# Kernel tuning notes

Hardware: AMD Instinct MI355X
Metric: run time of the kernel (lower is better)

## Reference

```python
import jax, jax.numpy as jnp
import numpy as np

B, S, D = 4, 2048, 1024

def setup_inputs() -> dict:
    key = jax.random.key(0)
    k1, k2, k3, k4 = jax.random.split(key, 4)
    scale = 1.0 / np.sqrt(D)  # roughly glorot-like magnitude for weights
    return {
        "inputs": jax.random.normal(k1, (B, S, D), dtype=jnp.float32),
        "W_query": jax.random.normal(k2, (D, D), dtype=jnp.float32) * scale,
        "W_key": jax.random.normal(k3, (D, D), dtype=jnp.float32) * scale,
        "W_value": jax.random.normal(k4, (D, D), dtype=jnp.float32) * scale,
    }

def reference(inputs, W_query, W_key, W_value):
    # QKV projections: [B,S,D] @ [D,D]
    q = jnp.einsum('bsd,de->bse', inputs, W_query)
    k = jnp.einsum('bsd,de->bse', inputs, W_key)
    v = jnp.einsum('bsd,de->bse', inputs, W_value)
    # Unscaled attention scores [B,S,S] (source applies no 1/sqrt(d))
    score = jnp.einsum('bqd,bkd->bqk', q, k)
    weights = jax.nn.softmax(score, axis=-1)
    context = jnp.einsum('bqk,bkd->bqd', weights, v)
    return context
```

## Files before the change

### kernel.cpp

```cpp
#include <hip/hip_runtime.h>
#include <math.h>


typedef __bf16 bf16;
typedef _Float16 f16;
typedef __bf16 bf16x8 __attribute__((ext_vector_type(8)));
typedef __bf16 bf16x4 __attribute__((ext_vector_type(4)));
typedef _Float16 f16x4 __attribute__((ext_vector_type(4)));
typedef _Float16 f16x8 __attribute__((ext_vector_type(8)));
typedef float  f32x4  __attribute__((ext_vector_type(4)));

template<typename E> struct vec8_of;
template<> struct vec8_of<bf16> { using type = bf16x8; };
template<> struct vec8_of<f16>  { using type = f16x8; };

__device__ inline f32x4 mfma16(bf16x8 a, bf16x8 b, f32x4 c) {
    return __builtin_amdgcn_mfma_f32_16x16x32_bf16(a, b, c, 0, 0, 0);
}
__device__ inline f32x4 mfma16(f16x8 a, f16x8 b, f32x4 c) {
    return __builtin_amdgcn_mfma_f32_16x16x32_f16(a, b, c, 0, 0, 0);
}

#define AS1 __attribute__((address_space(1)))
#define AS3 __attribute__((address_space(3)))

template<typename E>
__device__ inline void async_load16(const E* g, void* l) {
    __builtin_amdgcn_global_load_lds((const AS1 unsigned int*)g,
                                     (AS3 unsigned int*)l, 16, 0, 0);
}

template<typename E, bool SPLIT, int OUT_MODE, int BK>
__global__ __launch_bounds__(256) void gemm_bt(
    const E* __restrict__ Ahi, const E* __restrict__ Alo,
    const E* __restrict__ Bhi, const E* __restrict__ Blo,
    float* __restrict__ Cf, f16* __restrict__ Ch,
    bf16* __restrict__ Cbh, bf16* __restrict__ Cbl,
    int K, int lda, int ldb, int ldc,
    long long sA, long long sB, long long sC)
{
    using vec8 = typename vec8_of<E>::type;
    constexpr int NBUF = SPLIT ? 4 : 2;
    constexpr int TILE_BYTES = 128 * BK * (int)sizeof(E);
    constexpr int CPW = (TILE_BYTES / 1024) / 4;
    constexpr int SPR = (BK * (int)sizeof(E)) / 16;
    constexpr int SWZ = (SPR == 8) ? 7 : 0;
    constexpr int SMB = (OUT_MODE == 2) ? (128 * 130 * 2 > NBUF * TILE_BYTES
                                           ? 128 * 130 * 2 : NBUF * TILE_BYTES)
                                        : NBUF * TILE_BYTES;

    __shared__ __align__(16) char smraw[SMB];
    auto tr = (f16(*)[130])smraw;

    Ahi += (long long)blockIdx.z * sA;
    Bhi += (long long)blockIdx.z * sB;
    if (SPLIT) { Alo += (long long)blockIdx.z * sA; Blo += (long long)blockIdx.z * sB; }

    const int tid  = threadIdx.x;
    const int lane = tid & 63;
    const int wave = tid >> 6;
    const int quad = lane >> 4;
    const int l16  = lane & 15;
    const int wm   = (wave >> 1) * 64;
    const int wn   = (wave & 1) * 64;

    const long long rowA0 = (long long)blockIdx.y * 128;
    const long long colB0 = (long long)blockIdx.x * 128;

    int ofs[CPW], rr[CPW], cc8[CPW];
#pragma unroll
    for (int u = 0; u < CPW; u++) {
        ofs[u] = (wave * CPW + u) * 1024 + lane * 16;
        const int s = ofs[u] >> 4;
        rr[u]  = s / SPR;
        cc8[u] = (s & (SPR - 1)) ^ (rr[u] & SWZ);
    }

    f32x4 acc[4][4];
#pragma unroll
    for (int i = 0; i < 4; i++)
#pragma unroll
        for (int j = 0; j < 4; j++) acc[i][j] = (f32x4){0.f, 0.f, 0.f, 0.f};

    for (int k0 = 0; k0 < K; k0 += BK) {
#pragma unroll
        for (int u = 0; u < CPW; u++) {
            async_load16(Ahi + (rowA0 + rr[u]) * lda + k0 + cc8[u] * 8, smraw + 0 * TILE_BYTES + ofs[u]);
            async_load16(Bhi + (colB0 + rr[u]) * ldb + k0 + cc8[u] * 8, smraw + 1 * TILE_BYTES + ofs[u]);
            if (SPLIT) {
                async_load16(Alo + (rowA0 + rr[u]) * lda + k0 + cc8[u] * 8, smraw + 2 * TILE_BYTES + ofs[u]);
                async_load16(Blo + (colB0 + rr[u]) * ldb + k0 + cc8[u] * 8, smraw + 3 * TILE_BYTES + ofs[u]);
            }
        }
        __syncthreads();

#pragma unroll
        for (int kh = 0; kh < BK / 32; kh++) {
            const int kc8 = kh * 4 + quad;
            vec8 a_hi[4], b_hi[4], a_lo[4], b_lo[4];
#pragma unroll
            for (int i = 0; i < 4; i++) {
                const int ra = wm + i * 16 + l16;
                const int rb = wn + i * 16 + l16;
                const int oa = ra * (SPR * 16) + ((kc8 ^ (ra & SWZ)) << 4);
                const int ob = rb * (SPR * 16) + ((kc8 ^ (rb & SWZ)) << 4);
                a_hi[i] = *(const vec8*)(smraw + 0 * TILE_BYTES + oa);
                b_hi[i] = *(const vec8*)(smraw + 1 * TILE_BYTES + ob);
                if (SPLIT) {
                    a_lo[i] = *(const vec8*)(smraw + 2 * TILE_BYTES + oa);
                    b_lo[i] = *(const vec8*)(smraw + 3 * TILE_BYTES + ob);
                }
            }
#pragma unroll
            for (int i = 0; i < 4; i++)
#pragma unroll
                for (int j = 0; j < 4; j++) {
                    acc[i][j] = mfma16(a_hi[i], b_hi[j], acc[i][j]);
                    if (SPLIT) {
                        acc[i][j] = mfma16(a_hi[i], b_lo[j], acc[i][j]);
                        acc[i][j] = mfma16(a_lo[i], b_hi[j], acc[i][j]);
                    }
                }
        }
        __syncthreads();
    }

    if (OUT_MODE == 2) {
#pragma unroll
        for (int i = 0; i < 4; i++)
#pragma unroll
            for (int j = 0; j < 4; j++)
#pragma unroll
                for (int e = 0; e < 4; e++)
                    tr[wn + j * 16 + l16][wm + i * 16 + quad * 4 + e] = (f16)acc[i][j][e];
        __syncthreads();
        const int batch = (int)(rowA0 >> 11);
        const int rib   = (int)(rowA0 & 2047);
        const int c  = tid >> 1;
        const int r0 = (tid & 1) << 6;
        f16* vt = Ch + (long long)batch * 1024 * 2048 + (long long)(colB0 + c) * ldc + rib + r0;
#pragma unroll
        for (int u = 0; u < 64; u += 8)
            *(f16x8*)(vt + u) = *(const f16x8*)&tr[c][r0 + u];
        return;
    }

    const long long cOff = (long long)blockIdx.z * sC +
                           (rowA0 + wm + quad * 4) * (long long)ldc + colB0 + wn + l16;
#pragma unroll
    for (int i = 0; i < 4; i++)
#pragma unroll
        for (int e = 0; e < 4; e++) {
            const long long ro = cOff + (i * 16 + e) * ldc;
            if (OUT_MODE == 0) {
                float* rp = Cf + ro;
#pragma unroll
                for (int j = 0; j < 4; j++) rp[j * 16] = acc[i][j][e];
            } else if (OUT_MODE == 1) {
                f16* rp = Ch + ro;
#pragma unroll
                for (int j = 0; j < 4; j++) rp[j * 16] = (f16)acc[i][j][e];
            } else {
                bf16* rh = Cbh + ro;
                bf16* rl = Cbl + ro;
#pragma unroll
                for (int j = 0; j < 4; j++) {
                    float v = acc[i][j][e];
                    bf16 h = (bf16)v;
                    rh[j * 16] = h;
                    rl[j * 16] = (bf16)(v - (float)h);
                }
            }
        }
}

__global__ __launch_bounds__(256) void split_x(const float4* __restrict__ X,
                                               bf16* __restrict__ hi, bf16* __restrict__ lo,
                                               f16* __restrict__ xf,
                                               long long n4)
{
    long long i = (long long)blockIdx.x * 256 + threadIdx.x;
    if (i >= n4) return;
    float4 v = X[i];
    bf16 h0 = (bf16)v.x, h1 = (bf16)v.y, h2 = (bf16)v.z, h3 = (bf16)v.w;
    bf16x4 hv = {h0, h1, h2, h3};
    bf16x4 lv = {(bf16)(v.x - (float)h0), (bf16)(v.y - (float)h1),
                 (bf16)(v.z - (float)h2), (bf16)(v.w - (float)h3)};
    *(bf16x4*)(hi + 4 * i) = hv;
    *(bf16x4*)(lo + 4 * i) = lv;
    if (xf) {
        f16x4 fv = {(f16)v.x, (f16)v.y, (f16)v.z, (f16)v.w};
        *(f16x4*)(xf + 4 * i) = fv;
    }
}

__global__ __launch_bounds__(256) void split_w2(const float4* __restrict__ W0,
                                                const float4* __restrict__ W1,
                                                bf16* __restrict__ h0, bf16* __restrict__ l0,
                                                bf16* __restrict__ h1, bf16* __restrict__ l1,
                                                long long n4)
{
    long long i = (long long)blockIdx.x * 256 + threadIdx.x;
    if (i >= n4) return;
    const float4* W = blockIdx.z ? W1 : W0;
    bf16* hh = blockIdx.z ? h1 : h0;
    bf16* ll = blockIdx.z ? l1 : l0;
    float4 v = W[i];
    bf16 a0 = (bf16)v.x, a1 = (bf16)v.y, a2 = (bf16)v.z, a3 = (bf16)v.w;
    bf16x4 hv = {a0, a1, a2, a3};
    bf16x4 lv = {(bf16)(v.x - (float)a0), (bf16)(v.y - (float)a1),
                 (bf16)(v.z - (float)a2), (bf16)(v.w - (float)a3)};
    *(bf16x4*)(hh + 4 * i) = hv;
    *(bf16x4*)(ll + 4 * i) = lv;
}

__global__ __launch_bounds__(256) void wsplit_t(const float* __restrict__ W,
                                                bf16* __restrict__ Thi, bf16* __restrict__ Tlo,
                                                int R, int C)
{
    __shared__ float t[32][33];
    const int bx = blockIdx.x * 32, by = blockIdx.y * 32;
    const int tx = threadIdx.x & 31, ty = threadIdx.x >> 5;
#pragma unroll
    for (int i = 0; i < 32; i += 8)
        t[ty + i][tx] = W[(long long)(by + ty + i) * C + bx + tx];
    __syncthreads();
#pragma unroll
    for (int i = 0; i < 32; i += 8) {
        float v = t[tx][ty + i];
        long long o = (long long)(bx + ty + i) * R + by + tx;
        bf16 h = (bf16)v;
        Thi[o] = h;
        Tlo[o] = (bf16)(v - (float)h);
    }
}

__global__ __launch_bounds__(256) void softmax_f16(const float* __restrict__ S,
                                                   f16* __restrict__ P, int n)
{
    const long long row = blockIdx.x;
    const float* p = S + row * (long long)n;
    f16* q = P + row * (long long)n;
    const int tid = threadIdx.x;
    const int wv = tid >> 6, lane = tid & 63;

    float v[8];
    float m = -3.4e38f;
#pragma unroll
    for (int i = 0; i < 8; i++) { v[i] = p[tid + (i << 8)]; m = fmaxf(m, v[i]); }
#pragma unroll
    for (int off = 32; off > 0; off >>= 1) m = fmaxf(m, __shfl_xor(m, off, 64));

    __shared__ float red[4];
    if (lane == 0) red[wv] = m;
    __syncthreads();
    m = fmaxf(fmaxf(red[0], red[1]), fmaxf(red[2], red[3]));

    float s = 0.f;
#pragma unroll
    for (int i = 0; i < 8; i++) { v[i] = __expf(v[i] - m); s += v[i]; }
#pragma unroll
    for (int off = 32; off > 0; off >>= 1) s += __shfl_xor(s, off, 64);
    __syncthreads();
    if (lane == 0) red[wv] = s;
    __syncthreads();
    s = red[0] + red[1] + red[2] + red[3];

    const float inv = 1.0f / s;
#pragma unroll
    for (int i = 0; i < 8; i++) q[tid + (i << 8)] = (f16)(v[i] * inv);
}

extern "C" void kernel_launch(void* const* d_in, const int* in_sizes, int n_in,
                              void* d_out, int out_size, void* d_ws, size_t ws_size,
                              hipStream_t stream) {
    const float* X  = (const float*)d_in[0];
    const float* Wq = (const float*)d_in[1];
    const float* Wk = (const float*)d_in[2];
    const float* Wv = (const float*)d_in[3];
    float* out = (float*)d_out;

    const long long MD = 8192LL * 1024;
    const long long DD = 1024LL * 1024;

    char* w = (char*)d_ws;
    const long long MB = 1024LL * 1024;
    bf16* Xhi   = (bf16*)(w + 0 * MB);
    bf16* Xlo   = (bf16*)(w + 16 * MB);
    f16*  Xf    = (f16*) (w + 32 * MB);
    bf16* Wq_h  = (bf16*)(w + 48 * MB);
    bf16* Wq_l  = (bf16*)(w + 50 * MB);
    bf16* Wk_h  = (bf16*)(w + 52 * MB);
    bf16* Wk_l  = (bf16*)(w + 54 * MB);
    bf16* Wvt_h = (bf16*)(w + 56 * MB);
    bf16* Wvt_l = (bf16*)(w + 58 * MB);
    bf16* Mt_h  = (bf16*)(w + 60 * MB);
    bf16* Mt_l  = (bf16*)(w + 62 * MB);
    f16*  T     = (f16*) (w + 64 * MB);
    f16*  Vt    = (f16*) (w + 80 * MB);
    float* Sc   = (float*)(w + 96 * MB);
    f16*  P     = (f16*) (w + 160 * MB);

    dim3 blk(256);

    split_x<<<dim3((unsigned)(MD / 4 / 256)), blk, 0, stream>>>(
        (const float4*)X, Xhi, Xlo, Xf, MD / 4);

    split_w2<<<dim3((unsigned)(DD / 4 / 256), 1, 2), blk, 0, stream>>>(
        (const float4*)Wq, (const float4*)Wk, Wq_h, Wq_l, Wk_h, Wk_l, DD / 4);
    wsplit_t<<<dim3(32, 32, 1), blk, 0, stream>>>(Wv, Wvt_h, Wvt_l, 1024, 1024);

    gemm_bt<bf16, true, 3, 32><<<dim3(8, 8, 1), blk, 0, stream>>>(
        Wk_h, Wk_l, Wq_h, Wq_l, nullptr, nullptr, Mt_h, Mt_l,
        1024, 1024, 1024, 1024, 0, 0, 0);

    gemm_bt<bf16, true, 1, 32><<<dim3(8, 64, 1), blk, 0, stream>>>(
        Xhi, Xlo, Mt_h, Mt_l, nullptr, T, nullptr, nullptr,
        1024, 1024, 1024, 1024, 0, 0, 0);

    gemm_bt<bf16, false, 2, 64><<<dim3(8, 64, 1), blk, 0, stream>>>(
        Xhi, nullptr, Wvt_h, nullptr, nullptr, Vt, nullptr, nullptr,
        1024, 1024, 1024, 2048, 0, 0, 0);

    gemm_bt<f16, false, 0, 64><<<dim3(16, 16, 4), blk, 0, stream>>>(
        T, nullptr, Xf, nullptr, Sc, nullptr, nullptr, nullptr,
        1024, 1024, 1024, 2048,
        2048LL * 1024, 2048LL * 1024, 2048LL * 2048);

    softmax_f16<<<dim3(4 * 2048), blk, 0, stream>>>(Sc, P, 2048);

    gemm_bt<f16, false, 0, 64><<<dim3(8, 16, 4), blk, 0, stream>>>(
        P, nullptr, Vt, nullptr, out, nullptr, nullptr, nullptr,
        2048, 2048, 2048, 1024,
        2048LL * 2048, 1024LL * 2048, 2048LL * 1024);
}
```

Measured before the change: 339.2 us.

## Merge preprocessing and projection GEMMs into fewer combined kernel launches

Turns the GEMM kernel into a device function with explicit block indices and dynamic shared memory, then merges launches. The weight splits and the Wv transpose share one kernel, the X split shares one with the Wk·Wq^T GEMM, and the T and V projection GEMMs run as two z-slices of a single grid. This cuts launch count and lets the small Mt GEMM and the T/V GEMMs overlap with other work. In xsplit_mt the Mt GEMM blocks do not depend on the X split, so they can run concurrently. The tradeoff is that dynamic shared memory is sized for the largest variant, which may reduce occupancy for the smaller ones.

```diff
diff --git a/kernel.cpp b/kernel.cpp
--- a/kernel.cpp
+++ b/kernel.cpp
@@ -31,30 +31,25 @@
 }
 
 template<typename E, bool SPLIT, int OUT_MODE, int BK>
-__global__ __launch_bounds__(256) void gemm_bt(
+__device__ __forceinline__ void gemm_body(
+    char* __restrict__ smraw,
     const E* __restrict__ Ahi, const E* __restrict__ Alo,
     const E* __restrict__ Bhi, const E* __restrict__ Blo,
     float* __restrict__ Cf, f16* __restrict__ Ch,
     bf16* __restrict__ Cbh, bf16* __restrict__ Cbl,
     int K, int lda, int ldb, int ldc,
-    long long sA, long long sB, long long sC)
+    long long sA, long long sB, long long sC,
+    int bx, int by, int bz)
 {
     using vec8 = typename vec8_of<E>::type;
-    constexpr int NBUF = SPLIT ? 4 : 2;
     constexpr int TILE_BYTES = 128 * BK * (int)sizeof(E);
     constexpr int CPW = (TILE_BYTES / 1024) / 4;
     constexpr int SPR = (BK * (int)sizeof(E)) / 16;
     constexpr int SWZ = (SPR == 8) ? 7 : 0;
-    constexpr int SMB = (OUT_MODE == 2) ? (128 * 130 * 2 > NBUF * TILE_BYTES
-                                           ? 128 * 130 * 2 : NBUF * TILE_BYTES)
-                                        : NBUF * TILE_BYTES;
-
-    __shared__ __align__(16) char smraw[SMB];
-    auto tr = (f16(*)[130])smraw;
-
-    Ahi += (long long)blockIdx.z * sA;
-    Bhi += (long long)blockIdx.z * sB;
-    if (SPLIT) { Alo += (long long)blockIdx.z * sA; Blo += (long long)blockIdx.z * sB; }
+
+    Ahi += (long long)bz * sA;
+    Bhi += (long long)bz * sB;
+    if (SPLIT) { Alo += (long long)bz * sA; Blo += (long long)bz * sB; }
 
     const int tid  = threadIdx.x;
     const int lane = tid & 63;
@@ -64,8 +59,8 @@
     const int wm   = (wave >> 1) * 64;
     const int wn   = (wave & 1) * 64;
 
-    const long long rowA0 = (long long)blockIdx.y * 128;
-    const long long colB0 = (long long)blockIdx.x * 128;
+    const long long rowA0 = (long long)by * 128;
+    const long long colB0 = (long long)bx * 128;
 
     int ofs[CPW], rr[CPW], cc8[CPW];
 #pragma unroll
@@ -126,6 +121,7 @@
     }
 
     if (OUT_MODE == 2) {
+        auto tr = (f16(*)[130])smraw;
 #pragma unroll
         for (int i = 0; i < 4; i++)
 #pragma unroll
@@ -145,7 +141,7 @@
         return;
     }
 
-    const long long cOff = (long long)blockIdx.z * sC +
+    const long long cOff = (long long)bz * sC +
                            (rowA0 + wm + quad * 4) * (long long)ldc + colB0 + wn + l16;
 #pragma unroll
     for (int i = 0; i < 4; i++)
@@ -174,65 +170,106 @@
         }
 }
 
-__global__ __launch_bounds__(256) void split_x(const float4* __restrict__ X,
-                                               bf16* __restrict__ hi, bf16* __restrict__ lo,
-                                               f16* __restrict__ xf,
-                                               long long n4)
-{
-    long long i = (long long)blockIdx.x * 256 + threadIdx.x;
-    if (i >= n4) return;
-    float4 v = X[i];
-    bf16 h0 = (bf16)v.x, h1 = (bf16)v.y, h2 = (bf16)v.z, h3 = (bf16)v.w;
-    bf16x4 hv = {h0, h1, h2, h3};
-    bf16x4 lv = {(bf16)(v.x - (float)h0), (bf16)(v.y - (float)h1),
-                 (bf16)(v.z - (float)h2), (bf16)(v.w - (float)h3)};
-    *(bf16x4*)(hi + 4 * i) = hv;
-    *(bf16x4*)(lo + 4 * i) = lv;
-    if (xf) {
+__global__ __launch_bounds__(256) void prep_w(
+    const float* __restrict__ Wq, const float* __restrict__ Wk, const float* __restrict__ Wv,
+    bf16* __restrict__ Wq_h, bf16* __restrict__ Wq_l,
+    bf16* __restrict__ Wk_h, bf16* __restrict__ Wk_l,
+    bf16* __restrict__ Wvt_h, bf16* __restrict__ Wvt_l)
+{
+    int b = blockIdx.x;
+    if (b < 2048) {
+        const float4* W = (const float4*)(b < 1024 ? Wq : Wk);
+        bf16* hh = b < 1024 ? Wq_h : Wk_h;
+        bf16* ll = b < 1024 ? Wq_l : Wk_l;
+        long long i = (long long)(b & 1023) * 256 + threadIdx.x;
+        float4 v = W[i];
+        bf16 a0 = (bf16)v.x, a1 = (bf16)v.y, a2 = (bf16)v.z, a3 = (bf16)v.w;
+        bf16x4 hv = {a0, a1, a2, a3};
+        bf16x4 lv = {(bf16)(v.x - (float)a0), (bf16)(v.y - (float)a1),
+                     (bf16)(v.z - (float)a2), (bf16)(v.w - (float)a3)};
+        *(bf16x4*)(hh + 4 * i) = hv;
+        *(bf16x4*)(ll + 4 * i) = lv;
+    } else {
+        b -= 2048;
+        __shared__ float t[32][33];
+        const int bx = (b & 31) * 32, by = (b >> 5) * 32;
+        const int tx = threadIdx.x & 31, ty = threadIdx.x >> 5;
+#pragma unroll
+        for (int i = 0; i < 32; i += 8)
+            t[ty + i][tx] = Wv[(long long)(by + ty + i) * 1024 + bx + tx];
+        __syncthreads();
+#pragma unroll
+        for (int i = 0; i < 32; i += 8) {
+            float v = t[tx][ty + i];
+            long long o = (long long)(bx + ty + i) * 1024 + by + tx;
+            bf16 h = (bf16)v;
+            Wvt_h[o] = h;
+            Wvt_l[o] = (bf16)(v - (float)h);
+        }
+    }
+}
+
+__global__ __launch_bounds__(256) void xsplit_mt(
+    const float4* __restrict__ X,
+    bf16* __restrict__ Xhi, bf16* __restrict__ Xlo, f16* __restrict__ Xf,
+    const bf16* __restrict__ Wk_h, const bf16* __restrict__ Wk_l,
+    const bf16* __restrict__ Wq_h, const bf16* __restrict__ Wq_l,
+    bf16* __restrict__ Mt_h, bf16* __restrict__ Mt_l)
+{
+    extern __shared__ char smraw[];
+    int b = blockIdx.x;
+    if (b < 8192) {
+        long long i = (long long)b * 256 + threadIdx.x;
+        float4 v = X[i];
+        bf16 h0 = (bf16)v.x, h1 = (bf16)v.y, h2 = (bf16)v.z, h3 = (bf16)v.w;
+        bf16x4 hv = {h0, h1, h2, h3};
+        bf16x4 lv = {(bf16)(v.x - (float)h0), (bf16)(v.y - (float)h1),
+                     (bf16)(v.z - (float)h2), (bf16)(v.w - (float)h3)};
+        *(bf16x4*)(Xhi + 4 * i) = hv;
+        *(bf16x4*)(Xlo + 4 * i) = lv;
         f16x4 fv = {(f16)v.x, (f16)v.y, (f16)v.z, (f16)v.w};
-        *(f16x4*)(xf + 4 * i) = fv;
-    }
-}
-
-__global__ __launch_bounds__(256) void split_w2(const float4* __restrict__ W0,
-                                                const float4* __restrict__ W1,
-                                                bf16* __restrict__ h0, bf16* __restrict__ l0,
-                                                bf16* __restrict__ h1, bf16* __restrict__ l1,
-                                                long long n4)
-{
-    long long i = (long long)blockIdx.x * 256 + threadIdx.x;
-    if (i >= n4) return;
-    const float4* W = blockIdx.z ? W1 : W0;
-    bf16* hh = blockIdx.z ? h1 : h0;
-    bf16* ll = blockIdx.z ? l1 : l0;
-    float4 v = W[i];
-    bf16 a0 = (bf16)v.x, a1 = (bf16)v.y, a2 = (bf16)v.z, a3 = (bf16)v.w;
-    bf16x4 hv = {a0, a1, a2, a3};
-    bf16x4 lv = {(bf16)(v.x - (float)a0), (bf16)(v.y - (float)a1),
-                 (bf16)(v.z - (float)a2), (bf16)(v.w - (float)a3)};
-    *(bf16x4*)(hh + 4 * i) = hv;
-    *(bf16x4*)(ll + 4 * i) = lv;
-}
-
-__global__ __launch_bounds__(256) void wsplit_t(const float* __restrict__ W,
-                                                bf16* __restrict__ Thi, bf16* __restrict__ Tlo,
-                                                int R, int C)
-{
-    __shared__ float t[32][33];
-    const int bx = blockIdx.x * 32, by = blockIdx.y * 32;
-    const int tx = threadIdx.x & 31, ty = threadIdx.x >> 5;
-#pragma unroll
-    for (int i = 0; i < 32; i += 8)
-        t[ty + i][tx] = W[(long long)(by + ty + i) * C + bx + tx];
-    __syncthreads();
-#pragma unroll
-    for (int i = 0; i < 32; i += 8) {
-        float v = t[tx][ty + i];
-        long long o = (long long)(bx + ty + i) * R + by + tx;
-        bf16 h = (bf16)v;
-        Thi[o] = h;
-        Tlo[o] = (bf16)(v - (float)h);
-    }
+        *(f16x4*)(Xf + 4 * i) = fv;
+    } else {
+        b -= 8192;
+        gemm_body<bf16, true, 3, 32>(smraw, Wk_h, Wk_l, Wq_h, Wq_l,
+                                     nullptr, nullptr, Mt_h, Mt_l,
+                                     1024, 1024, 1024, 1024, 0, 0, 0,
+                                     b & 7, b >> 3, 0);
+    }
+}
+
+__global__ __launch_bounds__(256) void t_and_v(
+    const bf16* __restrict__ Xhi, const bf16* __restrict__ Xlo,
+    const bf16* __restrict__ Mt_h, const bf16* __restrict__ Mt_l,
+    const bf16* __restrict__ Wvt_h,
+    f16* __restrict__ T, f16* __restrict__ Vt)
+{
+    extern __shared__ char smraw[];
+    if (blockIdx.z == 0)
+        gemm_body<bf16, true, 1, 32>(smraw, Xhi, Xlo, Mt_h, Mt_l,
+                                     nullptr, T, nullptr, nullptr,
+                                     1024, 1024, 1024, 1024, 0, 0, 0,
+                                     blockIdx.x, blockIdx.y, 0);
+    else
+        gemm_body<bf16, false, 2, 64>(smraw, Xhi, nullptr, Wvt_h, nullptr,
+                                      nullptr, Vt, nullptr, nullptr,
+                                      1024, 1024, 1024, 2048, 0, 0, 0,
+                                      blockIdx.x, blockIdx.y, 0);
+}
+
+template<typename E, bool SPLIT, int OUT_MODE, int BK>
+__global__ __launch_bounds__(256) void gemm_bt(
+    const E* __restrict__ Ahi, const E* __restrict__ Alo,
+    const E* __restrict__ Bhi, const E* __restrict__ Blo,
+    float* __restrict__ Cf, f16* __restrict__ Ch,
+    bf16* __restrict__ Cbh, bf16* __restrict__ Cbl,
+    int K, int lda, int ldb, int ldc,
+    long long sA, long long sB, long long sC)
+{
+    extern __shared__ char smraw[];
+    gemm_body<E, SPLIT, OUT_MODE, BK>(smraw, Ahi, Alo, Bhi, Blo, Cf, Ch, Cbh, Cbl,
+                                      K, lda, ldb, ldc, sA, sB, sC,
+                                      blockIdx.x, blockIdx.y, blockIdx.z);
 }
 
 __global__ __launch_bounds__(256) void softmax_f16(const float* __restrict__ S,
@@ -279,9 +316,6 @@
     const float* Wk = (const float*)d_in[2];
     const float* Wv = (const float*)d_in[3];
     float* out = (float*)d_out;
-
-    const long long MD = 8192LL * 1024;
-    const long long DD = 1024LL * 1024;
 
     char* w = (char*)d_ws;
     const long long MB = 1024LL * 1024;
@@ -303,33 +337,23 @@
 
     dim3 blk(256);
 
-    split_x<<<dim3((unsigned)(MD / 4 / 256)), blk, 0, stream>>>(
-        (const float4*)X, Xhi, Xlo, Xf, MD / 4);
-
-    split_w2<<<dim3((unsigned)(DD / 4 / 256), 1, 2), blk, 0, stream>>>(
-        (const float4*)Wq, (const float4*)Wk, Wq_h, Wq_l, Wk_h, Wk_l, DD / 4);
-    wsplit_t<<<dim3(32, 32, 1), blk, 0, stream>>>(Wv, Wvt_h, Wvt_l, 1024, 1024);
-
-    gemm_bt<bf16, true, 3, 32><<<dim3(8, 8, 1), blk, 0, stream>>>(
-        Wk_h, Wk_l, Wq_h, Wq_l, nullptr, nullptr, Mt_h, Mt_l,
-        1024, 1024, 1024, 1024, 0, 0, 0);
-
-    gemm_bt<bf16, true, 1, 32><<<dim3(8, 64, 1), blk, 0, stream>>>(
-        Xhi, Xlo, Mt_h, Mt_l, nullptr, T, nullptr, nullptr,
-        1024, 1024, 1024, 1024, 0, 0, 0);
-
-    gemm_bt<bf16, false, 2, 64><<<dim3(8, 64, 1), blk, 0, stream>>>(
-        Xhi, nullptr, Wvt_h, nullptr, nullptr, Vt, nullptr, nullptr,
-        1024, 1024, 1024, 2048, 0, 0, 0);
-
-    gemm_bt<f16, false, 0, 64><<<dim3(16, 16, 4), blk, 0, stream>>>(
+    prep_w<<<dim3(3072), blk, 0, stream>>>(Wq, Wk, Wv,
+                                           Wq_h, Wq_l, Wk_h, Wk_l, Wvt_h, Wvt_l);
+
+    xsplit_mt<<<dim3(8192 + 64), blk, 32768, stream>>>(
+        (const float4*)X, Xhi, Xlo, Xf, Wk_h, Wk_l, Wq_h, Wq_l, Mt_h, Mt_l);
+
+    t_and_v<<<dim3(8, 64, 2), blk, 33280, stream>>>(
+        Xhi, Xlo, Mt_h, Mt_l, Wvt_h, T, Vt);
+
+    gemm_bt<f16, false, 0, 64><<<dim3(16, 16, 4), blk, 32768, stream>>>(
         T, nullptr, Xf, nullptr, Sc, nullptr, nullptr, nullptr,
         1024, 1024, 1024, 2048,
         2048LL * 1024, 2048LL * 1024, 2048LL * 2048);
 
     softmax_f16<<<dim3(4 * 2048), blk, 0, stream>>>(Sc, P, 2048);
 
-    gemm_bt<f16, false, 0, 64><<<dim3(8, 16, 4), blk, 0, stream>>>(
+    gemm_bt<f16, false, 0, 64><<<dim3(8, 16, 4), blk, 32768, stream>>>(
         P, nullptr, Vt, nullptr, out, nullptr, nullptr, nullptr,
         2048, 2048, 2048, 1024,
         2048LL * 2048, 1024LL * 2048, 2048LL * 1024);
```

New measurement: 349.3 us. 3.0% more time.
